# Performance work log

Hardware: AMD Instinct MI355X
Metric: run time of the kernel (lower is better)

## Reference

```python
import jax, jax.numpy as jnp
import numpy as np

B, H, W, C = 1, 64, 64, 256
HEADS, K, DIL = 8, 7, 2
HD = C // HEADS
FF = 4 * C
EPS = 1e-5
SCALE = 1.0 / float(np.sqrt(HD))


def _axis_indices(L, k, d):
    """NATTEN dilated neighborhood: per dilation-group clamped sliding window.
    Returns key indices [L,k] and relative-position-bias indices [L,k]."""
    i = np.arange(L)
    g, rem = i // d, i % d                      # position within dilation group
    lg = (L - rem + d - 1) // d                 # group length per position
    start = np.clip(g - k // 2, 0, lg - k)      # clamped window start (group coords)
    a = np.arange(k)
    kidx = (start[:, None] + a[None, :]) * d + rem[:, None]          # key coord
    bidx = start[:, None] + a[None, :] - g[:, None] + (k - 1)        # rpb coord in [0, 2k-2]
    return kidx.astype(np.int32), bidx.astype(np.int32)


def setup_inputs():
    key = jax.random.key(0)
    ks = jax.random.split(key, 8)
    p = lambda k_, sh: jax.random.normal(k_, sh, jnp.float32) * 0.02
    return {
        "x": jax.random.normal(ks[0], (B, H, W, C), jnp.float32),
        "ln1_g": jnp.ones((C,), jnp.float32), "ln1_b": jnp.zeros((C,), jnp.float32),
        "wq": p(ks[1], (C, C)), "bq": jnp.zeros((C,), jnp.float32),
        "wk": p(ks[2], (C, C)), "bk": jnp.zeros((C,), jnp.float32),
        "wv": p(ks[3], (C, C)), "bv": jnp.zeros((C,), jnp.float32),
        "rpb": p(ks[4], (HEADS, 2 * K - 1, 2 * K - 1)),
        "wo": p(ks[5], (C, C)), "bo": jnp.zeros((C,), jnp.float32),
        "ln2_g": jnp.ones((C,), jnp.float32), "ln2_b": jnp.zeros((C,), jnp.float32),
        "w1": p(ks[6], (C, FF)), "b1": jnp.zeros((FF,), jnp.float32),
        "w2": p(ks[7], (FF, C)), "b2": jnp.zeros((C,), jnp.float32),
    }


def _layer_norm(x, g, b):
    m = jnp.mean(x, -1, keepdims=True)
    v = jnp.mean(jnp.square(x - m), -1, keepdims=True)
    return (x - m) * jax.lax.rsqrt(v + EPS) * g + b


def reference(x, ln1_g, ln1_b, wq, bq, wk, bk, wv, bv, rpb, wo, bo,
              ln2_g, ln2_b, w1, b1, w2, b2):
    ih, bih = _axis_indices(H, K, DIL)   # [H,K]
    iw, biw = _axis_indices(W, K, DIL)   # [W,K]
    hs = _layer_norm(x, ln1_g, ln1_b)
    q = (hs @ wq + bq).reshape(B, H, W, HEADS, HD) * SCALE
    k = (hs @ wk + bk).reshape(B, H, W, HEADS, HD)
    v = (hs @ wv + bv).reshape(B, H, W, HEADS, HD)
    # gather dilated neighborhoods -> [B,H,W,K,K,heads,hd]
    k_nb = k[:, ih[:, None, :, None], iw[None, :, None, :], :, :]
    v_nb = v[:, ih[:, None, :, None], iw[None, :, None, :], :, :]
    # natten2dqkrpb: per-query scores over K*K dilated neighbors + rpb
    scores = jnp.einsum('bijnc,bijklnc->bnijkl', q, k_nb)
    bias = rpb[:, bih[:, None, :, None], biw[None, :, None, :]]  # [heads,H,W,K,K]
    scores = scores + bias[None]
    probs = jax.nn.softmax(scores.reshape(B, HEADS, H, W, K * K), axis=-1)
    # natten2dav
    ctx = jnp.einsum('bnijp,bijpnc->bijnc', probs,
                     v_nb.reshape(B, H, W, K * K, HEADS, HD))
    attn_out = ctx.reshape(B, H, W, C) @ wo + bo
    hs2 = x + attn_out                      # residual (layer_scale disabled: init 0.0)
    y = _layer_norm(hs2, ln2_g, ln2_b)
    y = jax.nn.gelu(y @ w1 + b1, approximate=False) @ w2 + b2
    return hs2 + y
```

## Files before the change

kernel.cpp:

```cpp
#include <hip/hip_runtime.h>
#include <math.h>

#define CC 256
#define NTOK 4096
#define NHEADS 8
#define HD 32
#define FFD 1024
#define LN_EPS 1e-5f
#define QSCALE 0.17677669529663687f

typedef __bf16 bf16x8 __attribute__((ext_vector_type(8)));
typedef float f32x4 __attribute__((ext_vector_type(4)));
typedef unsigned short u16x8 __attribute__((ext_vector_type(8)));

__device__ __forceinline__ unsigned short f2bf(float f) {
    unsigned u = __builtin_bit_cast(unsigned, f);
    u += 0x7fff + ((u >> 16) & 1);
    return (unsigned short)(u >> 16);
}
__device__ __forceinline__ float bf2f(unsigned short h) {
    unsigned u = ((unsigned)h) << 16;
    return __builtin_bit_cast(float, u);
}
__device__ __forceinline__ void gload16(const unsigned short* g, unsigned short* l) {
    __builtin_amdgcn_global_load_lds(
        (const __attribute__((address_space(1))) unsigned int*)(const void*)g,
        (__attribute__((address_space(3))) unsigned int*)(void*)l, 16, 0, 0);
}

__device__ __forceinline__ void ln_row(const float* __restrict__ x, const float* __restrict__ g,
                                       const float* __restrict__ b, unsigned short* __restrict__ out,
                                       int tok, int lane) {
    const float4 v = ((const float4*)(x + (size_t)tok * CC))[lane];
    float s  = v.x + v.y + v.z + v.w;
    float ss = v.x * v.x + v.y * v.y + v.z * v.z + v.w * v.w;
    #pragma unroll
    for (int o = 32; o > 0; o >>= 1) { s += __shfl_xor(s, o); ss += __shfl_xor(ss, o); }
    float m   = s * (1.0f / CC);
    float var = ss * (1.0f / CC) - m * m;
    float r   = rsqrtf(var + LN_EPS);
    float4 gv = ((const float4*)g)[lane];
    float4 bv = ((const float4*)b)[lane];
    ushort4 o4;
    o4.x = f2bf((v.x - m) * r * gv.x + bv.x);
    o4.y = f2bf((v.y - m) * r * gv.y + bv.y);
    o4.z = f2bf((v.z - m) * r * gv.z + bv.z);
    o4.w = f2bf((v.w - m) * r * gv.w + bv.w);
    ((ushort4*)(out + (size_t)tok * CC))[lane] = o4;
}

__global__ void ln_kernel(const float* __restrict__ x, const float* __restrict__ g,
                          const float* __restrict__ b, unsigned short* __restrict__ out) {
    ln_row(x, g, b, out, blockIdx.x * 4 + (threadIdx.x >> 6), threadIdx.x & 63);
}

__global__ void setup_kernel(const float* __restrict__ wq, const float* __restrict__ wk,
                             const float* __restrict__ wv, const float* __restrict__ wo,
                             const float* __restrict__ w1, const float* __restrict__ w2,
                             const float* __restrict__ bq, const float* __restrict__ bk,
                             const float* __restrict__ bv,
                             const float* __restrict__ x, const float* __restrict__ ln1_g,
                             const float* __restrict__ ln1_b,
                             unsigned short* __restrict__ wt_qkv, unsigned short* __restrict__ wo_t,
                             unsigned short* __restrict__ w1_t, unsigned short* __restrict__ w2_t,
                             float* __restrict__ bqkv, unsigned short* __restrict__ hs_bf) {
    int id = blockIdx.x;
    int t = threadIdx.x;
    if (id >= 193) {
        ln_row(x, ln1_g, ln1_b, hs_bf, (id - 193) * 4 + (t >> 6), t & 63);
        return;
    }
    if (id == 192) {
        bqkv[t]       = bq[t] * QSCALE;
        bqkv[256 + t] = bk[t];
        bqkv[512 + t] = bv[t];
        return;
    }
    const float* src; unsigned short* dst;
    int N, rowoff16 = 0, bx, by, KC = 8; float scale = 1.0f;
    if (id < 16)       { src = wq; dst = wt_qkv; N = 256;                  int l = id;       bx = l & 3;  by = l >> 2; scale = QSCALE; }
    else if (id < 32)  { src = wk; dst = wt_qkv; N = 256;  rowoff16 = 16;  int l = id - 16;  bx = l & 3;  by = l >> 2; }
    else if (id < 48)  { src = wv; dst = wt_qkv; N = 256;  rowoff16 = 32;  int l = id - 32;  bx = l & 3;  by = l >> 2; }
    else if (id < 64)  { src = wo; dst = wo_t;   N = 256;                  int l = id - 48;  bx = l & 3;  by = l >> 2; }
    else if (id < 128) { src = w1; dst = w1_t;   N = 1024;                 int l = id - 64;  bx = l & 15; by = l >> 4; }
    else               { src = w2; dst = w2_t;   N = 256;  KC = 32;        int l = id - 128; bx = l & 3;  by = l >> 2; }
    int n0 = bx * 64, k0 = by * 64;
    __shared__ float tile[64][65];
    int cc = t & 63, rb = t >> 6;
    #pragma unroll
    for (int i = 0; i < 16; i++) {
        int r = rb + i * 4;
        tile[r][cc] = src[(size_t)(k0 + r) * N + n0 + cc];
    }
    __syncthreads();
    int lane = t & 63, fr = lane & 15, sq = lane >> 4, ncl = t >> 6;
    #pragma unroll
    for (int kcl = 0; kcl < 2; kcl++) {
        unsigned short tmp[8];
        #pragma unroll
        for (int e = 0; e < 8; e++)
            tmp[e] = f2bf(tile[kcl * 32 + sq * 8 + e][ncl * 16 + fr] * scale);
        int nc = rowoff16 + (n0 >> 4) + ncl;
        int kc = (k0 >> 5) + kcl;
        *(u16x8*)(dst + ((size_t)(nc * KC + kc) * 64 + lane) * 8) = *(const u16x8*)tmp;
    }
}

template<int BM, int BN, int WARPS_M, int KD, int ACT, bool ADD_RES, bool OUT_BF16>
__global__ __launch_bounds__(256) void gemm_v3(
    const unsigned short* __restrict__ A, const unsigned short* __restrict__ Bf,
    const float* __restrict__ bias, const float* __restrict__ res,
    void* __restrict__ Cm, int N) {
    constexpr int WARPS_N = 4 / WARPS_M;
    constexpr int WM = BM / WARPS_M, WN = BN / WARPS_N;
    constexpr int MF = WM / 16, NF = WN / 16;
    constexpr int NIT = KD / 64;
    constexpr int KC = KD / 32;
    __shared__ unsigned short lds[2][BM * 64];
    const int t = threadIdx.x;
    const int lane = t & 63, w = t >> 6;
    const int wr = w / WARPS_N, wc = w % WARPS_N;
    const int bm = blockIdx.y * BM, bn = blockIdx.x * BN;
    const int fr = lane & 15, sq = lane >> 4;
    const int ncb = (bn >> 4) + wc * NF;

    auto stage = [&](int it, int buf) {
        unsigned short* La = lds[buf];
        #pragma unroll
        for (int i = 0; i < BM / 32; i++) {
            int c = t + i * 256;
            int s32 = c / (BM * 4), r = (c % (BM * 4)) >> 2, jj = c & 3;
            gload16(A + (size_t)(bm + r) * KD + it * 64 + s32 * 32 + jj * 8, La + c * 8);
        }
    };
    auto loadB = [&](bf16x8* bfrag, int s) {
        #pragma unroll
        for (int j = 0; j < NF; j++)
            bfrag[j] = *(const bf16x8*)(Bf + ((size_t)((ncb + j) * KC + s) * 64 + lane) * 8);
    };

    f32x4 acc[MF][NF] = {};
    bf16x8 bnext[NF];
    stage(0, 0);
    loadB(bnext, 0);
    for (int it = 0; it < NIT; ++it) {
        const int buf = it & 1;
        __syncthreads();
        if (it + 1 < NIT) stage(it + 1, buf ^ 1);
        #pragma unroll
        for (int kk = 0; kk < 2; kk++) {
            bf16x8 bcur[NF];
            #pragma unroll
            for (int j = 0; j < NF; j++) bcur[j] = bnext[j];
            int s = it * 2 + kk + 1;
            if (s < 2 * NIT) loadB(bnext, s);
            const char* La = (const char*)(lds[buf]) + kk * BM * 64;
            bf16x8 af[MF];
            #pragma unroll
            for (int i = 0; i < MF; i++)
                af[i] = *(const bf16x8*)(La + (wr * WM + i * 16 + fr) * 64 + sq * 16);
            #pragma unroll
            for (int i = 0; i < MF; i++)
                #pragma unroll
                for (int j = 0; j < NF; j++)
                    acc[i][j] = __builtin_amdgcn_mfma_f32_16x16x32_bf16(af[i], bcur[j], acc[i][j], 0, 0, 0);
        }
    }
    #pragma unroll
    for (int i = 0; i < MF; i++) {
        int row0 = bm + wr * WM + i * 16 + sq * 4;
        #pragma unroll
        for (int j = 0; j < NF; j++) {
            int col = bn + wc * WN + j * 16 + fr;
            float bvv = bias[col];
            #pragma unroll
            for (int r = 0; r < 4; r++) {
                float v = acc[i][j][r] + bvv;
                if constexpr (ACT == 1) v = 0.5f * v * (1.0f + erff(v * 0.70710678118654752f));
                if constexpr (ADD_RES) v += res[(size_t)(row0 + r) * N + col];
                if constexpr (OUT_BF16)
                    ((unsigned short*)Cm)[(size_t)(row0 + r) * N + col] = f2bf(v);
                else
                    ((float*)Cm)[(size_t)(row0 + r) * N + col] = v;
            }
        }
    }
}

__global__ __launch_bounds__(256) void attn_mfma(
    const unsigned short* __restrict__ qkv, const float* __restrict__ rpb,
    unsigned short* __restrict__ ctx) {
    __shared__ __align__(16) unsigned short VT[128][136];
    __shared__ __align__(16) unsigned short Pl[4][16][136];
    __shared__ unsigned short tbl[16][112];
    __shared__ float rpbl[4][172];

    const int t = threadIdx.x;
    const int lane = t & 63, w = t >> 6;
    const int fr = lane & 15, sq = lane >> 4;
    const int bid = blockIdx.x;
    const int p = bid & 3, tile = (bid >> 2) & 63, hb = bid >> 8;
    const int ri = p >> 1, rj = p & 1;
    const int tgi = (tile >> 3) * 4, tgj = (tile & 7) * 4;
    const int kgi0 = min(max(tgi - 3, 0), 22);
    const int kgj0 = min(max(tgj - 3, 0), 22);
    const int head = hb * 4 + w;

    for (int i = lane; i < 169; i += 64)
        rpbl[w][i] = rpb[head * 169 + i];
    if (lane == 0) rpbl[w][169] = -1e30f;

    for (int e = t; e < 16 * 112; e += 256) {
        int q = e / 112, kk = e % 112;
        unsigned short idx = 169;
        if (kk < 100) {
            int kr = kk / 10, kc = kk % 10;
            int qgi = tgi + (q >> 2), qgj = tgj + (q & 3);
            int kgi = kgi0 + kr, kgj = kgj0 + kc;
            int si = min(max(qgi - 3, 0), 25), sj = min(max(qgj - 3, 0), 25);
            if (kgi >= si && kgi <= si + 6 && kgj >= sj && kgj <= sj + 6)
                idx = (unsigned short)((kgi - qgi + 6) * 13 + (kgj - qgj + 6));
        }
        tbl[q][kk] = idx;
    }

    for (int c0 = t; c0 < 1600; c0 += 256) {
        int key = c0 >> 4, ch8 = c0 & 15;
        int kr = key / 10, kc = key % 10;
        int kt = ((kgi0 + kr) * 2 + ri) * 64 + (kgj0 + kc) * 2 + rj;
        u16x8 vv = *(const u16x8*)(qkv + (size_t)kt * 768 + 512 + hb * 128 + ch8 * 8);
        #pragma unroll
        for (int e = 0; e < 8; e++) VT[ch8 * 8 + e][key] = vv[e];
    }
    for (int c0 = t; c0 < 128 * 14; c0 += 256) {
        int row = c0 / 14, cp = c0 % 14;
        *(unsigned*)&VT[row][100 + cp * 2] = 0;
    }
    __syncthreads();

    const int qtok = ((tgi + (fr >> 2)) * 2 + ri) * 64 + (tgj + (fr & 3)) * 2 + rj;
    bf16x8 qf = *(const bf16x8*)(qkv + (size_t)qtok * 768 + head * 32 + sq * 8);

    f32x4 sc[7];
    #pragma unroll
    for (int c = 0; c < 7; c++) {
        int kk = c * 16 + fr;
        if (kk > 99) kk = 99;
        int kr = kk / 10, kc = kk % 10;
        int kt = ((kgi0 + kr) * 2 + ri) * 64 + (kgj0 + kc) * 2 + rj;
        bf16x8 kf = *(const bf16x8*)(qkv + (size_t)kt * 768 + 256 + head * 32 + sq * 8);
        f32x4 z = {0.0f, 0.0f, 0.0f, 0.0f};
        sc[c] = __builtin_amdgcn_mfma_f32_16x16x32_bf16(kf, qf, z, 0, 0, 0);
    }
    #pragma unroll
    for (int c = 0; c < 7; c++)
        #pragma unroll
        for (int r = 0; r < 4; r++) {
            int idx = tbl[fr][c * 16 + 4 * sq + r];
            sc[c][r] += rpbl[w][idx];
        }

    float mx = -1e30f;
    #pragma unroll
    for (int c = 0; c < 7; c++)
        #pragma unroll
        for (int r = 0; r < 4; r++) mx = fmaxf(mx, sc[c][r]);
    mx = fmaxf(mx, __shfl_xor(mx, 16));
    mx = fmaxf(mx, __shfl_xor(mx, 32));
    float sum = 0.0f;
    #pragma unroll
    for (int c = 0; c < 7; c++)
        #pragma unroll
        for (int r = 0; r < 4; r++) {
            sc[c][r] = __expf(sc[c][r] - mx);
            sum += sc[c][r];
        }
    sum += __shfl_xor(sum, 16);
    sum += __shfl_xor(sum, 32);
    float inv = 1.0f / sum;

    #pragma unroll
    for (int c = 0; c < 7; c++)
        #pragma unroll
        for (int r = 0; r < 4; r++)
            Pl[w][fr][c * 16 + 4 * sq + r] = f2bf(sc[c][r] * inv);
    *(unsigned long long*)&Pl[w][fr][112 + sq * 4] = 0ull;

    f32x4 o0 = {0, 0, 0, 0}, o1 = {0, 0, 0, 0};
    #pragma unroll
    for (int m = 0; m < 4; m++) {
        bf16x8 pf = *(const bf16x8*)(&Pl[w][fr][m * 32 + sq * 8]);
        bf16x8 v0 = *(const bf16x8*)(&VT[w * 32 + fr][m * 32 + sq * 8]);
        bf16x8 v1 = *(const bf16x8*)(&VT[w * 32 + 16 + fr][m * 32 + sq * 8]);
        o0 = __builtin_amdgcn_mfma_f32_16x16x32_bf16(pf, v0, o0, 0, 0, 0);
        o1 = __builtin_amdgcn_mfma_f32_16x16x32_bf16(pf, v1, o1, 0, 0, 0);
    }
    #pragma unroll
    for (int r = 0; r < 4; r++) {
        int tok = ((tgi + sq) * 2 + ri) * 64 + (tgj + r) * 2 + rj;
        ctx[(size_t)tok * 256 + head * 32 + fr]      = f2bf(o0[r]);
        ctx[(size_t)tok * 256 + head * 32 + 16 + fr] = f2bf(o1[r]);
    }
}

extern "C" void kernel_launch(void* const* d_in, const int* in_sizes, int n_in,
                              void* d_out, int out_size, void* d_ws, size_t ws_size,
                              hipStream_t stream) {
    const float* x     = (const float*)d_in[0];
    const float* ln1_g = (const float*)d_in[1];
    const float* ln1_b = (const float*)d_in[2];
    const float* wq    = (const float*)d_in[3];
    const float* bq    = (const float*)d_in[4];
    const float* wk    = (const float*)d_in[5];
    const float* bk    = (const float*)d_in[6];
    const float* wv    = (const float*)d_in[7];
    const float* bv    = (const float*)d_in[8];
    const float* rpb   = (const float*)d_in[9];
    const float* wo    = (const float*)d_in[10];
    const float* bo    = (const float*)d_in[11];
    const float* ln2_g = (const float*)d_in[12];
    const float* ln2_b = (const float*)d_in[13];
    const float* w1    = (const float*)d_in[14];
    const float* b1    = (const float*)d_in[15];
    const float* w2    = (const float*)d_in[16];
    const float* b2    = (const float*)d_in[17];

    char* wsb = (char*)d_ws;
    unsigned short* hs_bf  = (unsigned short*)(wsb);
    unsigned short* qkv_bf = (unsigned short*)(wsb + (2u << 20));
    unsigned short* ctx_bf = (unsigned short*)(wsb + (8u << 20));
    float*          hs2    = (float*)(wsb + (10u << 20));
    unsigned short* y1_bf  = (unsigned short*)(wsb + (14u << 20));
    unsigned short* gm_bf  = (unsigned short*)(wsb + (16u << 20));
    unsigned short* wt_qkv = (unsigned short*)(wsb + (24u << 20));
    unsigned short* wo_t   = wt_qkv + 768 * 256;
    unsigned short* w1_t   = wo_t + 256 * 256;
    unsigned short* w2_t   = w1_t + 1024 * 256;
    float*          bqkv   = (float*)(w2_t + 256 * 1024);

    setup_kernel<<<1217, 256, 0, stream>>>(wq, wk, wv, wo, w1, w2, bq, bk, bv,
                                           x, ln1_g, ln1_b,
                                           wt_qkv, wo_t, w1_t, w2_t, bqkv, hs_bf);
    gemm_v3<128, 64, 4, 256, 0, false, true><<<dim3(12, 32), 256, 0, stream>>>(
        hs_bf, wt_qkv, bqkv, nullptr, qkv_bf, 768);
    attn_mfma<<<512, 256, 0, stream>>>(qkv_bf, rpb, ctx_bf);
    gemm_v3<64, 64, 2, 256, 0, true, false><<<dim3(4, 64), 256, 0, stream>>>(
        ctx_bf, wo_t, bo, x, hs2, 256);
    ln_kernel<<<NTOK / 4, 256, 0, stream>>>(hs2, ln2_g, ln2_b, y1_bf);
    gemm_v3<128, 64, 4, 256, 1, false, true><<<dim3(16, 32), 256, 0, stream>>>(
        y1_bf, w1_t, b1, nullptr, gm_bf, 1024);
    gemm_v3<64, 64, 2, 1024, 0, true, false><<<dim3(4, 64), 256, 0, stream>>>(
        gm_bf, w2_t, b2, hs2, (float*)d_out, 256);
}
```

Baseline: 145.3 us.

## Restructure GEMM to stage full K-chunks of A and B in LDS with tile remapping

Replaces the double-buffered 64-wide K pipeline with a kernel that loads 256-wide K chunks of both A and the pre-fragmented B into LDS in MFMA fragment order, then runs all MFMAs from LDS. It adds an XCD-aware block index remap so neighbouring tiles land on the same chiplet for L2 reuse, and shrinks the tiles (64x64, 32x64 for the FFN down projection) to launch more workgroups. The aim is fewer per-step barriers, conflict-free fragment reads and better occupancy and cache locality. In exchange there is no overlap between loading a chunk and computing on it, and LDS use per block grows.

Result: no change. 142.7 us (-1.7%).

```diff
diff --git a/kernel.cpp b/kernel.cpp
--- a/kernel.cpp
+++ b/kernel.cpp
@@ -107,64 +107,62 @@
 }
 
 template<int BM, int BN, int WARPS_M, int KD, int ACT, bool ADD_RES, bool OUT_BF16>
-__global__ __launch_bounds__(256) void gemm_v3(
+__global__ __launch_bounds__(256) void gemm_fr(
     const unsigned short* __restrict__ A, const unsigned short* __restrict__ Bf,
     const float* __restrict__ bias, const float* __restrict__ res,
     void* __restrict__ Cm, int N) {
     constexpr int WARPS_N = 4 / WARPS_M;
     constexpr int WM = BM / WARPS_M, WN = BN / WARPS_N;
     constexpr int MF = WM / 16, NF = WN / 16;
-    constexpr int NIT = KD / 64;
+    constexpr int CHUNK = 256;
+    constexpr int NCH = KD / CHUNK;
+    constexpr int SC = CHUNK / 32;
     constexpr int KC = KD / 32;
-    __shared__ unsigned short lds[2][BM * 64];
-    const int t = threadIdx.x;
-    const int lane = t & 63, w = t >> 6;
+    constexpr int ACH = (BM / 16) * SC;
+    constexpr int BCH = (BN / 16) * SC;
+    __shared__ unsigned short lds[(BM + BN) * CHUNK];
+    unsigned short* La = lds;
+    unsigned short* Lb = lds + BM * CHUNK;
+    const int t = threadIdx.x, lane = t & 63, w = t >> 6;
     const int wr = w / WARPS_N, wc = w % WARPS_N;
-    const int bm = blockIdx.y * BM, bn = blockIdx.x * BN;
     const int fr = lane & 15, sq = lane >> 4;
-    const int ncb = (bn >> 4) + wc * NF;
-
-    auto stage = [&](int it, int buf) {
-        unsigned short* La = lds[buf];
-        #pragma unroll
-        for (int i = 0; i < BM / 32; i++) {
-            int c = t + i * 256;
-            int s32 = c / (BM * 4), r = (c % (BM * 4)) >> 2, jj = c & 3;
-            gload16(A + (size_t)(bm + r) * KD + it * 64 + s32 * 32 + jj * 8, La + c * 8);
-        }
-    };
-    auto loadB = [&](bf16x8* bfrag, int s) {
-        #pragma unroll
-        for (int j = 0; j < NF; j++)
-            bfrag[j] = *(const bf16x8*)(Bf + ((size_t)((ncb + j) * KC + s) * 64 + lane) * 8);
-    };
+    const int gx = gridDim.x;
+    const int nwg = gx * gridDim.y;
+    const int l0 = blockIdx.y * gx + blockIdx.x;
+    const int nl = (l0 & 7) * (nwg >> 3) + (l0 >> 3);
+    const int bm = (nl / gx) * BM, bn = (nl % gx) * BN;
 
     f32x4 acc[MF][NF] = {};
-    bf16x8 bnext[NF];
-    stage(0, 0);
-    loadB(bnext, 0);
-    for (int it = 0; it < NIT; ++it) {
-        const int buf = it & 1;
+    for (int ch = 0; ch < NCH; ++ch) {
+        #pragma unroll
+        for (int i = 0; i < ACH / 4; i++) {
+            int c = i * 4 + w, mc = c / SC, s = c % SC;
+            gload16(A + (size_t)(bm + mc * 16 + fr) * KD + ch * CHUNK + s * 32 + sq * 8,
+                    La + c * 512 + lane * 8);
+        }
+        #pragma unroll
+        for (int i = 0; i < BCH / 4; i++) {
+            int c = i * 4 + w, ncl = c / SC, s = c % SC;
+            gload16(Bf + ((size_t)(((bn >> 4) + ncl) * KC + ch * SC + s) * 64 + lane) * 8,
+                    Lb + c * 512 + lane * 8);
+        }
         __syncthreads();
-        if (it + 1 < NIT) stage(it + 1, buf ^ 1);
-        #pragma unroll
-        for (int kk = 0; kk < 2; kk++) {
-            bf16x8 bcur[NF];
-            #pragma unroll
-            for (int j = 0; j < NF; j++) bcur[j] = bnext[j];
-            int s = it * 2 + kk + 1;
-            if (s < 2 * NIT) loadB(bnext, s);
-            const char* La = (const char*)(lds[buf]) + kk * BM * 64;
-            bf16x8 af[MF];
+        #pragma unroll
+        for (int s = 0; s < SC; s++) {
+            bf16x8 af[MF], bfr[NF];
             #pragma unroll
             for (int i = 0; i < MF; i++)
-                af[i] = *(const bf16x8*)(La + (wr * WM + i * 16 + fr) * 64 + sq * 16);
+                af[i] = *(const bf16x8*)(La + ((wr * MF + i) * SC + s) * 512 + lane * 8);
+            #pragma unroll
+            for (int j = 0; j < NF; j++)
+                bfr[j] = *(const bf16x8*)(Lb + ((wc * NF + j) * SC + s) * 512 + lane * 8);
             #pragma unroll
             for (int i = 0; i < MF; i++)
                 #pragma unroll
                 for (int j = 0; j < NF; j++)
-                    acc[i][j] = __builtin_amdgcn_mfma_f32_16x16x32_bf16(af[i], bcur[j], acc[i][j], 0, 0, 0);
-        }
+                    acc[i][j] = __builtin_amdgcn_mfma_f32_16x16x32_bf16(af[i], bfr[j], acc[i][j], 0, 0, 0);
+        }
+        if (ch + 1 < NCH) __syncthreads();
     }
     #pragma unroll
     for (int i = 0; i < MF; i++) {
@@ -341,14 +339,14 @@
     setup_kernel<<<1217, 256, 0, stream>>>(wq, wk, wv, wo, w1, w2, bq, bk, bv,
                                            x, ln1_g, ln1_b,
                                            wt_qkv, wo_t, w1_t, w2_t, bqkv, hs_bf);
-    gemm_v3<128, 64, 4, 256, 0, false, true><<<dim3(12, 32), 256, 0, stream>>>(
+    gemm_fr<64, 64, 2, 256, 0, false, true><<<dim3(12, 64), 256, 0, stream>>>(
         hs_bf, wt_qkv, bqkv, nullptr, qkv_bf, 768);
     attn_mfma<<<512, 256, 0, stream>>>(qkv_bf, rpb, ctx_bf);
-    gemm_v3<64, 64, 2, 256, 0, true, false><<<dim3(4, 64), 256, 0, stream>>>(
+    gemm_fr<64, 64, 2, 256, 0, true, false><<<dim3(4, 64), 256, 0, stream>>>(
         ctx_bf, wo_t, bo, x, hs2, 256);
     ln_kernel<<<NTOK / 4, 256, 0, stream>>>(hs2, ln2_g, ln2_b, y1_bf);
-    gemm_v3<128, 64, 4, 256, 1, false, true><<<dim3(16, 32), 256, 0, stream>>>(
+    gemm_fr<64, 64, 2, 256, 1, false, true><<<dim3(16, 64), 256, 0, stream>>>(
         y1_bf, w1_t, b1, nullptr, gm_bf, 1024);
-    gemm_v3<64, 64, 2, 1024, 0, true, false><<<dim3(4, 64), 256, 0, stream>>>(
+    gemm_fr<32, 64, 1, 1024, 0, true, false><<<dim3(4, 128), 256, 0, stream>>>(
         gm_bf, w2_t, b2, hs2, (float*)d_out, 256);
 }
```
